# Kernel tuning notes

Hardware: AMD Instinct MI355X
Metric: run time of the kernel (lower is better)

Reference implementation:

```python
import jax, jax.numpy as jnp
import numpy as np

B, M, RPI = 16, 80, 256            # images, objects/image, relations/image
N, R = B * M, B * RPI
DF, REP, EMB, HID, NH, L = 12544, 1024, 256, 512, 8, 4
OBJC, RELC = 151, 51
IMW, IMH = 800.0, 600.0


def _ln(x, g, b):
    m = x.mean(-1, keepdims=True)
    v = ((x - m) ** 2).mean(-1, keepdims=True)
    return (x - m) * jax.lax.rsqrt(v + 1e-5) * g + b


def _encoder(x, qkv_w, qkv_b, out_w, out_b, f1_w, f1_b, f2_w, f2_b, ln1_s, ln1_b, ln2_s, ln2_b):
    # post-LN transformer encoder, L layers, x: [B, M, HID]
    Bb, Mm, D = x.shape
    dk = D // NH
    scale = 1.0 / jnp.sqrt(jnp.float32(dk))
    for l in range(L):
        qkv = x @ qkv_w[l].T + qkv_b[l]
        q, k, v = jnp.split(qkv, 3, axis=-1)
        hs = lambda t: t.reshape(Bb, Mm, NH, dk).transpose(0, 2, 1, 3)
        q, k, v = hs(q), hs(k), hs(v)
        att = jax.nn.softmax(jnp.einsum('bhqd,bhkd->bhqk', q, k) * scale, axis=-1)
        o = jnp.einsum('bhqk,bhkd->bhqd', att, v).transpose(0, 2, 1, 3).reshape(Bb, Mm, D)
        x = _ln(x + o @ out_w[l].T + out_b[l], ln1_s[l], ln1_b[l])
        f = jax.nn.relu(x @ f1_w[l].T + f1_b[l]) @ f2_w[l].T + f2_b[l]
        x = _ln(x + f, ln2_s[l], ln2_b[l])
    return x


def _box_info(boxes):
    wh = boxes[:, 2:] - boxes[:, :2] + 1.0
    xy = boxes[:, :2] + 0.5 * wh
    w, h = wh[:, :1], wh[:, 1:]
    x, y = xy[:, :1], xy[:, 1:]
    x1, y1, x2, y2 = boxes[:, 0:1], boxes[:, 1:2], boxes[:, 2:3], boxes[:, 3:4]
    return jnp.concatenate([w / IMW, h / IMH, x / IMW, y / IMH, x1 / IMW, y1 / IMH,
                            x2 / IMW, y2 / IMH, w * h / (IMW * IMH)], axis=-1)  # [N, 9]


def setup_inputs() -> dict:
    key = jax.random.key(0)
    ks = iter(jax.random.split(key, 80))
    nrm = lambda shape, s=0.02: jax.random.normal(next(ks), shape, jnp.float32) * s
    d = {}
    d['features'] = jax.random.normal(next(ks), (N, DF), jnp.float32)
    d['union_features'] = jax.random.normal(next(ks), (R, REP), jnp.float32)
    x1 = jax.random.uniform(next(ks), (N, 1)) * (IMW - 120.0)
    y1 = jax.random.uniform(next(ks), (N, 1)) * (IMH - 120.0)
    w = jax.random.uniform(next(ks), (N, 1)) * 100.0 + 5.0
    h = jax.random.uniform(next(ks), (N, 1)) * 100.0 + 5.0
    d['boxes'] = jnp.concatenate([x1, y1, x1 + w, y1 + h], axis=-1)
    d['logits'] = jax.random.normal(next(ks), (N, OBJC), jnp.float32)
    d['labels'] = jax.random.randint(next(ks), (N,), 0, OBJC)
    d['rel_pair_idxs'] = jax.random.randint(next(ks), (B, RPI, 2), 0, M)
    # feature extractor
    d['fe1_w'] = nrm((REP, DF)); d['fe1_b'] = jnp.zeros((REP,))
    d['fe2_w'] = nrm((REP, REP)); d['fe2_b'] = jnp.zeros((REP,))
    # embeddings
    d['emb1'] = nrm((OBJC, EMB), 1.0)
    d['emb2'] = nrm((OBJC, EMB), 1.0)
    # bbox embed 9->32->128
    d['bb1_w'] = nrm((32, 9)); d['bb1_b'] = jnp.zeros((32,))
    d['bb2_w'] = nrm((128, 32)); d['bb2_b'] = jnp.zeros((128,))
    d['lobj_w'] = nrm((HID, REP + EMB + 128)); d['lobj_b'] = jnp.zeros((HID,))
    d['ledge_w'] = nrm((HID, EMB + HID)); d['ledge_b'] = jnp.zeros((HID,))
    for p in ('o', 'e'):
        d[p + 'qkv_w'] = nrm((L, 3 * HID, HID)); d[p + 'qkv_b'] = jnp.zeros((L, 3 * HID))
        d[p + 'out_w'] = nrm((L, HID, HID)); d[p + 'out_b'] = jnp.zeros((L, HID))
        d[p + 'f1_w'] = nrm((L, HID, HID)); d[p + 'f1_b'] = jnp.zeros((L, HID))
        d[p + 'f2_w'] = nrm((L, HID, HID)); d[p + 'f2_b'] = jnp.zeros((L, HID))
        d[p + 'ln1_s'] = jnp.ones((L, HID)); d[p + 'ln1_b'] = jnp.zeros((L, HID))
        d[p + 'ln2_s'] = jnp.ones((L, HID)); d[p + 'ln2_b'] = jnp.zeros((L, HID))
    d['pcat_w'] = nrm((REP, 2 * HID)); d['pcat_b'] = jnp.zeros((REP,))
    d['fuse_w'] = nrm((REP, REP + HID)); d['fuse_b'] = jnp.zeros((REP,))
    d['cpx_w'] = nrm((RELC, 2 * REP)); d['cpx_b'] = jnp.zeros((RELC,))
    d['dpath_w'] = nrm((RELC, REP)); d['dpath_b'] = jnp.zeros((RELC,))
    return d


def reference(features, union_features, boxes, logits,
              fe1_w, fe1_b, fe2_w, fe2_b, emb1, emb2,
              bb1_w, bb1_b, bb2_w, bb2_b, lobj_w, lobj_b, ledge_w, ledge_b,
              oqkv_w, oqkv_b, oout_w, oout_b, of1_w, of1_b, of2_w, of2_b,
              oln1_s, oln1_b, oln2_s, oln2_b,
              eqkv_w, eqkv_b, eout_w, eout_b, ef1_w, ef1_b, ef2_w, ef2_b,
              eln1_s, eln1_b, eln2_s, eln2_b,
              pcat_w, pcat_b, fuse_w, fuse_b, cpx_w, cpx_b, dpath_w, dpath_b,
              labels, rel_pair_idxs):
    # FeatureExtractor
    bf = jax.nn.relu(features @ fe1_w.T + fe1_b)
    bf = jax.nn.relu(bf @ fe2_w.T + fe2_b)                        # [N, REP]
    # bbox embedding (dropout = identity in eval)
    pos = jax.nn.relu(_box_info(boxes) @ bb1_w.T + bb1_b)
    pos = jax.nn.relu(pos @ bb2_w.T + bb2_b)                      # [N, 128]
    obj_rep = jnp.concatenate([bf, emb1[labels], pos], -1) @ lobj_w.T + lobj_b  # [N, HID]
    obj_emb = _encoder(obj_rep.reshape(B, M, HID), oqkv_w, oqkv_b, oout_w, oout_b,
                       of1_w, of1_b, of2_w, of2_b, oln1_s, oln1_b, oln2_s, oln2_b)  # [B, M, HID]
    edge_in = jnp.concatenate([obj_emb.reshape(N, HID), emb2[labels]], -1) @ ledge_w.T + ledge_b
    gctx = _encoder(edge_in.reshape(B, M, HID), eqkv_w, eqkv_b, eout_w, eout_b,
                    ef1_w, ef1_b, ef2_w, ef2_b, eln1_s, eln1_b, eln2_s, eln2_b).mean(axis=1)  # [B, HID]
    # pair gather per image
    head = jax.vmap(lambda e, i: e[i])(obj_emb, rel_pair_idxs[:, :, 0])  # [B, RPI, HID]
    tail = jax.vmap(lambda e, i: e[i])(obj_emb, rel_pair_idxs[:, :, 1])
    pair = jnp.concatenate([head, tail], -1).reshape(R, 2 * HID)
    local = pair @ pcat_w.T + pcat_b                               # [R, REP]
    gexp = jnp.repeat(gctx, RPI, axis=0)                           # [R, HID]
    sem = jax.nn.relu(jnp.concatenate([local, gexp], -1) @ fuse_w.T + fuse_b)
    final = jnp.concatenate([sem, union_features], -1)             # [R, 2*REP]
    rel_logits = final @ cpx_w.T + cpx_b + local @ dpath_w.T + dpath_b  # [R, RELC]
    return rel_logits
```

## Files before the change

kernel.cpp:

```cpp
#include <hip/hip_runtime.h>
#include <hip/hip_bf16.h>
#include <cstdint>

#define DEV_INLINE __device__ __forceinline__

using u16 = unsigned short;
typedef __attribute__((ext_vector_type(8))) short bf8_t;
typedef __attribute__((ext_vector_type(4))) float f32x4;

constexpr int cB = 16, cM = 80, cRPI = 256;
constexpr int cN = cB * cM;
constexpr int cR = cB * cRPI;
constexpr int cDF = 12544, cREP = 1024, cEMB = 256, cHID = 512, cNH = 8, cL = 4;
constexpr int cRELC = 51;

DEV_INLINE u16 f2bf(float x) { return __builtin_bit_cast(u16, __float2bfloat16(x)); }
DEV_INLINE float bf2f(u16 u) { return __bfloat162float(__builtin_bit_cast(__hip_bfloat16, u)); }

DEV_INLINE float wave_max(float v) {
#pragma unroll
  for (int o = 32; o; o >>= 1) v = fmaxf(v, __shfl_xor(v, o));
  return v;
}
DEV_INLINE float wave_sum(float v) {
#pragma unroll
  for (int o = 32; o; o >>= 1) v += __shfl_xor(v, o);
  return v;
}

DEV_INLINE void xcd_remap(int& bx, int& by) {
  const int gx = gridDim.x;
  const int nwg = gx * gridDim.y;
  const int id = blockIdx.x + gx * blockIdx.y;
  const int q = nwg >> 3, r = nwg & 7;
  const int x = id & 7, k = id >> 3;
  const int idp = (x < r) ? x * (q + 1) + k : r * (q + 1) + (x - r) * q + k;
  bx = idp % gx;
  by = idp / gx;
}

template <int KK>
__global__ __launch_bounds__(256) void gemm_k1(
    const u16* __restrict__ A, int lda,
    const u16* __restrict__ Bw, int ldb,
    float* __restrict__ outF, int ldc,
    u16* __restrict__ outH, int ldh,
    const float* __restrict__ bias,
    const float* __restrict__ res, int resld, int resmode,
    int relu)
{
  constexpr int GR = KK / 8;
  constexpr int CH = 32 * GR;
  __shared__ u16 As[32 * KK];
  __shared__ u16 Bs[32 * KK];
  const int tid = threadIdx.x;
  const int wid = tid >> 6, lane = tid & 63;
  const int l15 = lane & 15, l4 = lane >> 4;
  int bx, by;
  xcd_remap(bx, by);
  const int bm = by * 32, bn = bx * 32;
  const int wr = wid >> 1, wc = wid & 1;

#pragma unroll
  for (int i = 0; i < CH / 256; ++i) {
    const int c = i * 256 + tid;
    const int row = c / GR, gran = c % GR;
    const int sg = gran ^ (row & 7);
    const u16* gp = A + (size_t)(bm + row) * lda + sg * 8;
    __builtin_amdgcn_global_load_lds(
        (const __attribute__((address_space(1))) void*)gp,
        (__attribute__((address_space(3))) void*)((char*)As + (size_t)(i * 256 + wid * 64) * 16),
        16, 0, 0);
  }
#pragma unroll
  for (int i = 0; i < CH / 256; ++i) {
    const int c = i * 256 + tid;
    const int row = c / GR, gran = c % GR;
    const int sg = gran ^ (row & 7);
    const u16* gp = Bw + (size_t)(bn + row) * ldb + sg * 8;
    __builtin_amdgcn_global_load_lds(
        (const __attribute__((address_space(1))) void*)gp,
        (__attribute__((address_space(3))) void*)((char*)Bs + (size_t)(i * 256 + wid * 64) * 16),
        16, 0, 0);
  }
  __syncthreads();

  const int ra = wr * 16 + l15;
  const int rb = wc * 16 + l15;
  f32x4 acc = {};
#pragma unroll
  for (int ks = 0; ks < KK / 32; ++ks) {
    const int ga = ((ks << 2) | l4) ^ (ra & 7);
    const int gb = ((ks << 2) | l4) ^ (rb & 7);
    const bf8_t af = *(const bf8_t*)&As[ra * KK + ga * 8];
    const bf8_t bv = *(const bf8_t*)&Bs[rb * KK + gb * 8];
    acc = __builtin_amdgcn_mfma_f32_16x16x32_bf16(af, bv, acc, 0, 0, 0);
  }

  const int ccol = bn + wc * 16 + l15;
  const float bv = bias ? bias[ccol] : 0.f;
#pragma unroll
  for (int g = 0; g < 4; ++g) {
    const int r = bm + wr * 16 + l4 * 4 + g;
    float v = acc[g] + bv;
    if (resmode == 1) v += res[(size_t)r * resld + ccol];
    else if (resmode == 2) v += res[(size_t)(r >> 8) * resld + ccol];
    if (relu) v = fmaxf(v, 0.f);
    if (outF) outF[(size_t)r * ldc + ccol] = v;
    if (outH) outH[(size_t)r * ldh + ccol] = f2bf(v);
  }
}

static void g512(hipStream_t s, const u16* A, int lda, const u16* W, int ldb,
                 int M, int N, float* outF, int ldc, u16* outH, int ldh,
                 const float* bias, const float* res, int resld, int resmode, int relu) {
  dim3 g(N / 32, M / 32);
  gemm_k1<512><<<g, 256, 0, s>>>(A, lda, W, ldb, outF, ldc, outH, ldh,
                                 bias, res, resld, resmode, relu);
}

template <int BM, int BN, bool SPLIT>
__global__ __launch_bounds__(256) void gemm_h(
    const u16* __restrict__ A, int lda,
    const u16* __restrict__ Bw, int ldb,
    int Mr, int Nr, int Klen,
    float* __restrict__ outF, int ldc,
    u16* __restrict__ outH, int ldh,
    const float* __restrict__ bias,
    const float* __restrict__ res, int resld, int resmode,
    int relu)
{
  constexpr int MF = BM > 32 ? BM / 32 : 1, NF = BN > 32 ? BN / 32 : 1;
  constexpr int ACH = BM * 4, BCH = BN * 4;
  __shared__ u16 As[2][BM * 32];
  __shared__ u16 Bs[2][BN * 32];
  const int tid = threadIdx.x;
  const int wid = tid >> 6, lane = tid & 63;
  const int l15 = lane & 15, l4 = lane >> 4;
  int bx, by;
  xcd_remap(bx, by);
  const int bm = by * BM, bn = bx * BN;
  const int wr = wid >> 1, wc = wid & 1;
  const int kbase = SPLIT ? blockIdx.z * Klen : 0;

  f32x4 acc[MF][NF] = {};

  auto stage = [&](int buf, int ks) {
    const int k0 = kbase + (ks << 5);
#pragma unroll
    for (int i = 0; i < (ACH + 255) / 256; ++i) {
      const int cA = i * 256 + tid;
      if (ACH % 256 == 0 || cA < ACH) {
        const int row = cA >> 2, seg = cA & 3;
        const int sseg = seg ^ (row & 3);
        const u16* gp = A + (size_t)(bm + row) * lda + k0 + sseg * 8;
        __builtin_amdgcn_global_load_lds(
            (const __attribute__((address_space(1))) void*)gp,
            (__attribute__((address_space(3))) void*)((char*)As[buf] + (size_t)(cA - lane) * 16),
            16, 0, 0);
      }
    }
#pragma unroll
    for (int i = 0; i < (BCH + 255) / 256; ++i) {
      const int cBp = i * 256 + ((tid + 128) & 255);
      if (BCH % 256 == 0 || cBp < BCH) {
        const int row = cBp >> 2, seg = cBp & 3;
        const int sseg = seg ^ (row & 3);
        int brow = bn + row; if (brow > Nr - 1) brow = Nr - 1;
        const u16* gp = Bw + (size_t)brow * ldb + k0 + sseg * 8;
        __builtin_amdgcn_global_load_lds(
            (const __attribute__((address_space(1))) void*)gp,
            (__attribute__((address_space(3))) void*)((char*)Bs[buf] + (size_t)(cBp - lane) * 16),
            16, 0, 0);
      }
    }
  };

  const int nk = Klen >> 5;
  stage(0, 0);
  __syncthreads();

  for (int ks = 0; ks < nk; ++ks) {
    const int cur = ks & 1;
    if (ks + 1 < nk) stage(cur ^ 1, ks + 1);

    bf8_t af[MF], bfr[NF];
#pragma unroll
    for (int m = 0; m < MF; ++m) {
      const int r = wr * (BM / 2) + m * 16 + l15;
      const int g = l4 ^ (r & 3);
      af[m] = *(const bf8_t*)&As[cur][r * 32 + g * 8];
    }
#pragma unroll
    for (int n = 0; n < NF; ++n) {
      const int r = wc * (BN / 2) + n * 16 + l15;
      const int g = l4 ^ (r & 3);
      bfr[n] = *(const bf8_t*)&Bs[cur][r * 32 + g * 8];
    }
#pragma unroll
    for (int m = 0; m < MF; ++m)
#pragma unroll
      for (int n = 0; n < NF; ++n)
        acc[m][n] = __builtin_amdgcn_mfma_f32_16x16x32_bf16(af[m], bfr[n], acc[m][n], 0, 0, 0);
    __syncthreads();
  }

  if (SPLIT) {
    float* po = outF + (size_t)blockIdx.z * Mr * ldc;
#pragma unroll
    for (int m = 0; m < MF; ++m)
#pragma unroll
      for (int n = 0; n < NF; ++n) {
        const int ccol = bn + wc * (BN / 2) + n * 16 + l15;
        if (ccol >= Nr) continue;
#pragma unroll
        for (int g = 0; g < 4; ++g) {
          const int r = bm + wr * (BM / 2) + m * 16 + l4 * 4 + g;
          po[(size_t)r * ldc + ccol] = acc[m][n][g];
        }
      }
  } else {
#pragma unroll
    for (int m = 0; m < MF; ++m)
#pragma unroll
      for (int n = 0; n < NF; ++n) {
        const int ccol = bn + wc * (BN / 2) + n * 16 + l15;
        if (ccol >= Nr) continue;
        const float bv = bias ? bias[ccol] : 0.f;
#pragma unroll
        for (int g = 0; g < 4; ++g) {
          const int r = bm + wr * (BM / 2) + m * 16 + l4 * 4 + g;
          float v = acc[m][n][g] + bv;
          if (resmode == 1) v += res[(size_t)r * resld + ccol];
          else if (resmode == 2) v += res[(size_t)(r >> 8) * resld + ccol];
          if (relu) v = fmaxf(v, 0.f);
          if (outF) outF[(size_t)r * ldc + ccol] = v;
          if (outH) outH[(size_t)r * ldh + ccol] = f2bf(v);
        }
      }
  }
}

template <int BM, int BN>
static void g16(hipStream_t s, const u16* A, int lda, const u16* W, int ldb,
                int M, int N, int K, float* outF, int ldc, u16* outH, int ldh,
                const float* bias, const float* res, int resld, int resmode, int relu) {
  dim3 g((N + BN - 1) / BN, M / BM);
  gemm_h<BM, BN, false><<<g, 256, 0, s>>>(A, lda, W, ldb, M, N, K, outF, ldc, outH, ldh,
                                          bias, res, resld, resmode, relu);
}

__global__ void conv_big2(const float* __restrict__ f, const float* __restrict__ w,
                          u16* __restrict__ fh, u16* __restrict__ wh) {
  constexpr int N1 = cN * cDF / 4;
  constexpr int N2 = cREP * cDF / 4;
  for (int i = blockIdx.x * 256 + threadIdx.x; i < N1 + N2; i += gridDim.x * 256) {
    const float4 v = (i < N1) ? ((const float4*)f)[i] : ((const float4*)w)[i - N1];
    ushort4 o = {f2bf(v.x), f2bf(v.y), f2bf(v.z), f2bf(v.w)};
    if (i < N1) ((ushort4*)fh)[i] = o; else ((ushort4*)wh)[i - N1] = o;
  }
}

constexpr size_t W_FE2 = 0, W_LOBJ = W_FE2 + 1048576, W_LEDGE = W_LOBJ + 720896,
  W_OQKV = W_LEDGE + 393216, W_OOUT = W_OQKV + 3145728, W_OF1 = W_OOUT + 1048576,
  W_OF2 = W_OF1 + 1048576, W_EQKV = W_OF2 + 1048576, W_EOUT = W_EQKV + 3145728,
  W_EF1 = W_EOUT + 1048576, W_EF2 = W_EF1 + 1048576, W_PCAT = W_EF2 + 1048576,
  W_FUSE = W_PCAT + 1048576, W_WEND = W_FUSE + 1572864;

struct EncSrcs {
  const float *fe2, *lobj, *ledge, *oqkv, *oout, *of1, *of2,
              *eqkv, *eout, *ef1, *ef2, *pcat, *fuse;
};

__global__ void conv_enc(EncSrcs S, u16* __restrict__ wb) {
#define SEG(nm, OFF, PRE, LEN) \
  if (i < (PRE) + (LEN)) { \
    const float4 v = ((const float4*)S.nm)[i - (PRE)]; \
    ushort4 o = {f2bf(v.x), f2bf(v.y), f2bf(v.z), f2bf(v.w)}; \
    ((ushort4*)(wb + (OFF)))[i - (PRE)] = o; \
  } else
  for (int i = blockIdx.x * 256 + threadIdx.x; i < (int)(W_WEND / 4); i += gridDim.x * 256) {
    SEG(fe2,  W_FE2,   0,       262144)
    SEG(lobj, W_LOBJ,  262144,  180224)
    SEG(ledge,W_LEDGE, 442368,  98304)
    SEG(oqkv, W_OQKV,  540672,  786432)
    SEG(oout, W_OOUT,  1327104, 262144)
    SEG(of1,  W_OF1,   1589248, 262144)
    SEG(of2,  W_OF2,   1851392, 262144)
    SEG(eqkv, W_EQKV,  2113536, 786432)
    SEG(eout, W_EOUT,  2899968, 262144)
    SEG(ef1,  W_EF1,   3162112, 262144)
    SEG(ef2,  W_EF2,   3424256, 262144)
    SEG(pcat, W_PCAT,  3686400, 262144)
    SEG(fuse, W_FUSE,  3948544, 393216)
    { }
  }
#undef SEG
}

__global__ void conv_cat(const float* __restrict__ cpx, const float* __restrict__ dpath,
                         const float* __restrict__ cb, const float* __restrict__ db,
                         u16* __restrict__ catw, float* __restrict__ biasc) {
  constexpr int N1 = cRELC * 512;
  constexpr int N2 = cRELC * 256;
  const int i0 = blockIdx.x * 256 + threadIdx.x;
  if (blockIdx.x == 0 && threadIdx.x < cRELC) biasc[threadIdx.x] = cb[threadIdx.x] + db[threadIdx.x];
  for (int i = i0; i < N1 + N2; i += gridDim.x * 256) {
    if (i < N1) {
      const int r = i >> 9, c = i & 511;
      const float4 v = ((const float4*)cpx)[i];
      ushort4 o = {f2bf(v.x), f2bf(v.y), f2bf(v.z), f2bf(v.w)};
      ((ushort4*)catw)[r * 768 + c] = o;
    } else {
      const int j = i - N1, r = j >> 8, c = j & 255;
      const float4 v = ((const float4*)dpath)[j];
      ushort4 o = {f2bf(v.x), f2bf(v.y), f2bf(v.z), f2bf(v.w)};
      ((ushort4*)catw)[r * 768 + 512 + c] = o;
    }
  }
}

__global__ void conv2d_kernel(const float* __restrict__ src, int slda,
                              u16* __restrict__ dst, int dld, int cols) {
  const int r = blockIdx.x;
  for (int c = threadIdx.x; c < cols; c += blockDim.x)
    dst[(size_t)r * dld + c] = f2bf(src[(size_t)r * slda + c]);
}

__global__ __launch_bounds__(256) void prep_obj(
    const float* __restrict__ boxes,
    const float* __restrict__ bb1w, const float* __restrict__ bb1b,
    const float* __restrict__ bb2w, const float* __restrict__ bb2b,
    const float* __restrict__ emb1, const int* __restrict__ labels,
    u16* __restrict__ obj_in) {
  __shared__ float W1[288];
  __shared__ float W2[4096];
  __shared__ float P1[8][33];
  const int tid = threadIdx.x;
  for (int i = tid; i < 288; i += 256) W1[i] = bb1w[i];
  for (int i = tid; i < 4096; i += 256) W2[i] = bb2w[i];
  __syncthreads();
  const int r8 = tid >> 5, sub = tid & 31;
  const int row = blockIdx.x * 8 + r8;
  const float x1 = boxes[row * 4], y1 = boxes[row * 4 + 1];
  const float x2 = boxes[row * 4 + 2], y2 = boxes[row * 4 + 3];
  const float w = x2 - x1 + 1.f, h = y2 - y1 + 1.f;
  const float bi[9] = {w / 800.f, h / 600.f, (x1 + 0.5f * w) / 800.f, (y1 + 0.5f * h) / 600.f,
                       x1 / 800.f, y1 / 600.f, x2 / 800.f, y2 / 600.f, w * h / 480000.f};
  float p = bb1b[sub];
#pragma unroll
  for (int j = 0; j < 9; ++j) p += bi[j] * W1[sub * 9 + j];
  P1[r8][sub] = fmaxf(p, 0.f);
  __syncthreads();
#pragma unroll
  for (int jo = 0; jo < 4; ++jo) {
    const int o = sub + jo * 32;
    float a = bb2b[o];
#pragma unroll
    for (int j2 = 0; j2 < 32; ++j2) a += P1[r8][j2] * W2[o * 32 + j2];
    obj_in[(size_t)row * 1408 + 1280 + o] = f2bf(fmaxf(a, 0.f));
  }
  const int l = labels[row];
#pragma unroll
  for (int k = 0; k < 8; ++k)
    obj_in[(size_t)row * 1408 + 1024 + sub + k * 32] = f2bf(emb1[(size_t)l * 256 + sub + k * 32]);
}

__global__ void gather_emb_h(const float* __restrict__ emb, const int* __restrict__ labels,
                             u16* __restrict__ dst, int dld) {
  const int i = blockIdx.x;
  const int l = labels[i];
  const float* s = emb + (size_t)l * cEMB;
  for (int c = threadIdx.x; c < cEMB; c += blockDim.x)
    dst[(size_t)i * dld + c] = f2bf(s[c]);
}

__global__ __launch_bounds__(256) void attn_kernel(const u16* __restrict__ qkv,
                                                   u16* __restrict__ o) {
  __shared__ float Ks[80][65];
  __shared__ float Vs[80][65];
  const int bh = blockIdx.x;
  const int b = bh >> 3, h = bh & 7;
  const int tid = threadIdx.x;
  const u16* base = qkv + (size_t)(b * cM) * 1536 + h * 64;

  for (int e = tid; e < 640; e += 256) {
    const int r = e >> 3, d0 = (e & 7) * 8;
    const bf8_t kv = *(const bf8_t*)&base[(size_t)r * 1536 + 512 + d0];
    const bf8_t vv = *(const bf8_t*)&base[(size_t)r * 1536 + 1024 + d0];
#pragma unroll
    for (int j = 0; j < 8; ++j) {
      Ks[r][d0 + j] = bf2f((u16)kv[j]);
      Vs[r][d0 + j] = bf2f((u16)vv[j]);
    }
  }
  __syncthreads();

  const int wave = tid >> 6, lane = tid & 63;
  const int r0 = blockIdx.y * 16;
  for (int r = r0 + wave; r < r0 + 16; r += 4) {
    const float qd = bf2f(base[(size_t)r * 1536 + lane]);
    const int c2 = 64 + lane;
    const int c2c = (c2 < 80) ? c2 : 0;
    float s0 = 0.f, s1 = 0.f;
#pragma unroll 8
    for (int d = 0; d < 64; ++d) {
      const float qv = __shfl(qd, d);
      s0 += qv * Ks[lane][d];
      s1 += qv * Ks[c2c][d];
    }
    s0 *= 0.125f;
    s1 = (c2 < 80) ? s1 * 0.125f : -1e30f;
    const float mx = wave_max(fmaxf(s0, s1));
    const float p0 = __expf(s0 - mx);
    const float p1 = (c2 < 80) ? __expf(s1 - mx) : 0.f;
    const float ssum = wave_sum(p0 + p1);

    float od = 0.f;
#pragma unroll 8
    for (int c = 0; c < 64; ++c) od += __shfl(p0, c) * Vs[c][lane];
#pragma unroll
    for (int c = 0; c < 16; ++c) od += __shfl(p1, c) * Vs[64 + c][lane];
    od /= ssum;
    o[(size_t)(b * cM + r) * cHID + h * 64 + lane] = f2bf(od);
  }
}

__global__ __launch_bounds__(256) void ln_kernel(
    const float* __restrict__ in, float* __restrict__ outF,
    u16* __restrict__ outH, int ldh,
    const float* __restrict__ g, const float* __restrict__ bta) {
  const int row = blockIdx.x * 4 + (threadIdx.x >> 6);
  const int lane = threadIdx.x & 63;
  const float* x = in + (size_t)row * cHID;
  float v[8];
  float s = 0.f;
#pragma unroll
  for (int i = 0; i < 8; ++i) { v[i] = x[lane + i * 64]; s += v[i]; }
  s = wave_sum(s);
  const float mean = s * (1.f / 512.f);
  float vs = 0.f;
#pragma unroll
  for (int i = 0; i < 8; ++i) { const float d = v[i] - mean; vs += d * d; }
  vs = wave_sum(vs);
  const float inv = rsqrtf(vs * (1.f / 512.f) + 1e-5f);
#pragma unroll
  for (int i = 0; i < 8; ++i) {
    const int c = lane + i * 64;
    const float y = (v[i] - mean) * inv * g[c] + bta[c];
    outF[(size_t)row * cHID + c] = y;
    outH[(size_t)row * ldh + c] = f2bf(y);
  }
}

__global__ void mean_kernel(const float* __restrict__ x, u16* __restrict__ gctx_h) {
  const int b = blockIdx.x;
  const int c = threadIdx.x;
  float s = 0.f;
  for (int m = 0; m < cM; ++m) s += x[(size_t)(b * cM + m) * cHID + c];
  gctx_h[(size_t)b * cHID + c] = f2bf(s * (1.f / 80.f));
}

__global__ void pair_gather_h(const u16* __restrict__ obj, int old, const int* __restrict__ idx,
                              u16* __restrict__ pair) {
  const int r = blockIdx.x;
  const int b = r >> 8, rr = r & 255;
  const int i0 = idx[(size_t)(b * cRPI + rr) * 2 + 0];
  const int i1 = idx[(size_t)(b * cRPI + rr) * 2 + 1];
  const u16* hsrc = obj + (size_t)(b * cM + i0) * old;
  const u16* tsrc = obj + (size_t)(b * cM + i1) * old;
  u16* p = pair + (size_t)r * 1024;
  for (int c = threadIdx.x; c < cHID; c += blockDim.x) {
    p[c] = hsrc[c];
    p[cHID + c] = tsrc[c];
  }
}

__global__ void reduce8_kernel(const float* __restrict__ p, const float* __restrict__ bias,
                               u16* __restrict__ outH) {
  const int idx = blockIdx.x * 256 + threadIdx.x;
  constexpr int total = cN * cREP;
  if (idx >= total) return;
  float v = bias[idx & 1023];
#pragma unroll
  for (int z = 0; z < 8; ++z) v += p[(size_t)z * total + idx];
  outH[idx] = f2bf(fmaxf(v, 0.f));
}

__global__ void freduce_kernel(const float* __restrict__ p, const float* __restrict__ biasc,
                               float* __restrict__ out) {
  const int idx = blockIdx.x * 256 + threadIdx.x;
  if (idx >= cR * cRELC) return;
  const int r = idx / cRELC, c = idx - r * cRELC;
  float v = biasc[c];
#pragma unroll
  for (int z = 0; z < 4; ++z) v += p[(size_t)z * cR * 64 + (size_t)r * 64 + c];
  out[idx] = v;
}

static void run_encoder(hipStream_t s, float* x, u16* xh, u16* qkvh, u16* attn_h,
                        float* res1, u16* f_h,
                        const u16* qkvw, const float* qkvb,
                        const u16* outw, const float* outb,
                        const u16* f1w, const float* f1b,
                        const u16* f2w, const float* f2b,
                        const float* ln1s, const float* ln1b,
                        const float* ln2s, const float* ln2b,
                        u16* last_bf, int last_ld) {
  for (int l = 0; l < cL; ++l) {
    g512(s, xh, 512, qkvw + (size_t)l * 1536 * 512, 512, cN, 1536,
         nullptr, 0, qkvh, 1536, qkvb + l * 1536, nullptr, 0, 0, 0);
    attn_kernel<<<dim3(cB * cNH, 5), 256, 0, s>>>(qkvh, attn_h);
    g512(s, attn_h, 512, outw + (size_t)l * 512 * 512, 512, cN, 512,
         res1, 512, nullptr, 0, outb + l * 512, x, 512, 1, 0);
    ln_kernel<<<cN / 4, 256, 0, s>>>(res1, x, xh, 512, ln1s + l * 512, ln1b + l * 512);
    g512(s, xh, 512, f1w + (size_t)l * 512 * 512, 512, cN, 512,
         nullptr, 0, f_h, 512, f1b + l * 512, nullptr, 0, 0, 1);
    g512(s, f_h, 512, f2w + (size_t)l * 512 * 512, 512, cN, 512,
         res1, 512, nullptr, 0, f2b + l * 512, x, 512, 1, 0);
    const bool last = (l == cL - 1);
    ln_kernel<<<cN / 4, 256, 0, s>>>(res1, x, last ? last_bf : xh, last ? last_ld : 512,
                                     ln2s + l * 512, ln2b + l * 512);
  }
}

constexpr size_t OFF_FEAT  = 0;
constexpr size_t OFF_FE1W  = 32112640;
constexpr size_t OFF_PART  = 57802752;
constexpr size_t P_END     = 99745792;
constexpr size_t OFF_PAIR  = 0;
constexpr size_t OFF_FINAL = 8388608;
constexpr size_t OFF_OBJIN = 33554432;
constexpr size_t OFF_QKVH  = 37158912;
constexpr size_t OFF_X     = 41091072;
constexpr size_t OFF_XH    = 43712512;
constexpr size_t OFF_ATTN  = 45023232;
constexpr size_t OFF_RES   = 46333952;
constexpr size_t OFF_FH    = 48955392;
constexpr size_t OFF_EDGE  = 50266112;

extern "C" void kernel_launch(void* const* d_in, const int* in_sizes, int n_in,
                              void* d_out, int out_size, void* d_ws, size_t ws_size,
                              hipStream_t stream) {
  (void)in_sizes; (void)n_in; (void)out_size; (void)ws_size;

  const float* features = (const float*)d_in[0];
  const float* unionf   = (const float*)d_in[1];
  const float* boxes    = (const float*)d_in[2];
  const int*   labels   = (const int*)d_in[4];
  const int*   relidx   = (const int*)d_in[5];
  const float* fe1_w = (const float*)d_in[6];
  const float* fe1_b = (const float*)d_in[7];
  const float* fe2_w = (const float*)d_in[8];
  const float* fe2_b = (const float*)d_in[9];
  const float* emb1  = (const float*)d_in[10];
  const float* emb2  = (const float*)d_in[11];
  const float* bb1_w = (const float*)d_in[12];
  const float* bb1_b = (const float*)d_in[13];
  const float* bb2_w = (const float*)d_in[14];
  const float* bb2_b = (const float*)d_in[15];
  const float* lobj_w = (const float*)d_in[16];
  const float* lobj_b = (const float*)d_in[17];
  const float* ledge_w = (const float*)d_in[18];
  const float* ledge_b = (const float*)d_in[19];
  const float* oqkv_w = (const float*)d_in[20];
  const float* oqkv_b = (const float*)d_in[21];
  const float* oout_w = (const float*)d_in[22];
  const float* oout_b = (const float*)d_in[23];
  const float* of1_w = (const float*)d_in[24];
  const float* of1_b = (const float*)d_in[25];
  const float* of2_w = (const float*)d_in[26];
  const float* of2_b = (const float*)d_in[27];
  const float* oln1_s = (const float*)d_in[28];
  const float* oln1_b = (const float*)d_in[29];
  const float* oln2_s = (const float*)d_in[30];
  const float* oln2_b = (const float*)d_in[31];
  const float* eqkv_w = (const float*)d_in[32];
  const float* eqkv_b = (const float*)d_in[33];
  const float* eout_w = (const float*)d_in[34];
  const float* eout_b = (const float*)d_in[35];
  const float* ef1_w = (const float*)d_in[36];
  const float* ef1_b = (const float*)d_in[37];
  const float* ef2_w = (const float*)d_in[38];
  const float* ef2_b = (const float*)d_in[39];
  const float* eln1_s = (const float*)d_in[40];
  const float* eln1_b = (const float*)d_in[41];
  const float* eln2_s = (const float*)d_in[42];
  const float* eln2_b = (const float*)d_in[43];
  const float* pcat_w = (const float*)d_in[44];
  const float* pcat_b = (const float*)d_in[45];
  const float* fuse_w = (const float*)d_in[46];
  const float* fuse_b = (const float*)d_in[47];
  const float* cpx_w  = (const float*)d_in[48];
  const float* cpx_b  = (const float*)d_in[49];
  const float* dpath_w = (const float*)d_in[50];
  const float* dpath_b = (const float*)d_in[51];

  char* wsb = (char*)d_ws;
  u16* feat_h  = (u16*)(wsb + OFF_FEAT);
  u16* fe1w_h  = (u16*)(wsb + OFF_FE1W);
  float* part  = (float*)(wsb + OFF_PART);
  u16* pair    = (u16*)(wsb + OFF_PAIR);
  u16* finalb  = (u16*)(wsb + OFF_FINAL);
  u16* obj_in  = (u16*)(wsb + OFF_OBJIN);
  u16* qkvh    = (u16*)(wsb + OFF_QKVH);
  float* x     = (float*)(wsb + OFF_X);
  u16* xh      = (u16*)(wsb + OFF_XH);
  u16* attn_h  = (u16*)(wsb + OFF_ATTN);
  float* res1  = (float*)(wsb + OFF_RES);
  u16* f_h     = (u16*)(wsb + OFF_FH);
  u16* edge_in = (u16*)(wsb + OFF_EDGE);

  size_t off = P_END;
  auto alloc = [&](size_t bytes) { char* p = wsb + off; off = (off + bytes + 255) & ~(size_t)255; return p; };
  u16* wblock   = (u16*)alloc(W_WEND * 2);
  u16* catw     = (u16*)alloc(313344);
  float* biasc  = (float*)alloc(256);
  u16* bf0h     = (u16*)alloc(2621440);
  u16* gctx_h   = (u16*)alloc(65536);
  float* gcproj = (float*)alloc(262144);
  float* fpart  = (float*)alloc(4194304);

  const u16* fe2w_h   = wblock + W_FE2;
  const u16* lobjw_h  = wblock + W_LOBJ;
  const u16* ledgew_h = wblock + W_LEDGE;
  const u16* oqkvw_h  = wblock + W_OQKV;
  const u16* ooutw_h  = wblock + W_OOUT;
  const u16* of1w_h   = wblock + W_OF1;
  const u16* of2w_h   = wblock + W_OF2;
  const u16* eqkvw_h  = wblock + W_EQKV;
  const u16* eoutw_h  = wblock + W_EOUT;
  const u16* ef1w_h   = wblock + W_EF1;
  const u16* ef2w_h   = wblock + W_EF2;
  const u16* pcatw_h  = wblock + W_PCAT;
  const u16* fusew_h  = wblock + W_FUSE;

  conv_big2<<<2048, 256, 0, stream>>>(features, fe1_w, feat_h, fe1w_h);
  EncSrcs es = {fe2_w, lobj_w, ledge_w, oqkv_w, oout_w, of1_w, of2_w,
                eqkv_w, eout_w, ef1_w, ef2_w, pcat_w, fuse_w};
  conv_enc<<<2048, 256, 0, stream>>>(es, wblock);
  conv_cat<<<160, 256, 0, stream>>>(cpx_w, dpath_w, cpx_b, dpath_b, catw, biasc);

  gemm_h<128, 128, true><<<dim3(8, 10, 8), 256, 0, stream>>>(
      feat_h, cDF, fe1w_h, cDF, cN, cREP, cDF / 8, part, cREP,
      nullptr, 0, nullptr, nullptr, 0, 0, 0);
  reduce8_kernel<<<(cN * cREP + 255) / 256, 256, 0, stream>>>(part, fe1_b, bf0h);

  prep_obj<<<cN / 8, 256, 0, stream>>>(boxes, bb1_w, bb1_b, bb2_w, bb2_b, emb1, labels, obj_in);

  g16<32, 32>(stream, bf0h, 1024, fe2w_h, 1024, cN, cREP, cREP,
              nullptr, 0, obj_in, 1408, fe2_b, nullptr, 0, 0, 1);

  g16<32, 32>(stream, obj_in, 1408, lobjw_h, 1408, cN, cHID, 1408,
              x, 512, xh, 512, lobj_b, nullptr, 0, 0, 0);

  run_encoder(stream, x, xh, qkvh, attn_h, res1, f_h,
              oqkvw_h, oqkv_b, ooutw_h, oout_b, of1w_h, of1_b, of2w_h, of2_b,
              oln1_s, oln1_b, oln2_s, oln2_b, edge_in, 768);

  gather_emb_h<<<cN, 256, 0, stream>>>(emb2, labels, edge_in + 512, 768);
  pair_gather_h<<<cR, 256, 0, stream>>>(edge_in, 768, relidx, pair);

  g16<32, 32>(stream, edge_in, 768, ledgew_h, 768, cN, cHID, 768,
              x, 512, xh, 512, ledge_b, nullptr, 0, 0, 0);
  run_encoder(stream, x, xh, qkvh, attn_h, res1, f_h,
              eqkvw_h, eqkv_b, eoutw_h, eout_b, ef1w_h, ef1_b, ef2w_h, ef2_b,
              eln1_s, eln1_b, eln2_s, eln2_b, xh, 512);
  mean_kernel<<<cB, cHID, 0, stream>>>(x, gctx_h);

  g512(stream, gctx_h, 512, fusew_h + 1024, 1536, 64, cREP,
       gcproj, 1024, nullptr, 0, fuse_b, nullptr, 0, 0, 0);

  conv2d_kernel<<<cR, 256, 0, stream>>>(unionf, 1024, finalb + 1024, 3072, 1024);
  g16<128, 64>(stream, pair, 1024, pcatw_h, 1024, cR, cREP, 1024,
               nullptr, 0, finalb + 2048, 3072, pcat_b, nullptr, 0, 0, 0);
  g16<128, 64>(stream, finalb + 2048, 3072, fusew_h, 1536, cR, cREP, 1024,
               nullptr, 0, finalb, 3072, nullptr, gcproj, 1024, 2, 1);

  gemm_h<64, 64, true><<<dim3(1, 64, 4), 256, 0, stream>>>(
      finalb, 3072, catw, 3072, cR, cRELC, 3072 / 4, fpart, 64,
      nullptr, 0, nullptr, nullptr, 0, 0, 0);
  freduce_kernel<<<(cR * cRELC + 255) / 256, 256, 0, stream>>>(fpart, biasc, (float*)d_out);
}
```

Baseline: 879.7 us.

## Fuse encoder out-proj, LN1, FFN, LN2 and next-layer QKV into one kernel

Replaces the per-layer sequence of out-projection GEMM, two LayerNorm kernels, two FFN GEMMs and the next layer's QKV GEMM with a single enc_tail kernel. Each block owns 32 full rows and keeps activations in LDS across the chained GEMMs, computing LayerNorm stats in-register. This removes several launches and round trips of intermediates through global memory. In exchange only 40 blocks run, each streaming all weights, so it has far less parallelism than the separate tiled GEMMs.

```diff
diff --git a/kernel.cpp b/kernel.cpp
--- a/kernel.cpp
+++ b/kernel.cpp
@@ -26,6 +26,12 @@
 #pragma unroll
   for (int o = 32; o; o >>= 1) v += __shfl_xor(v, o);
   return v;
+}
+
+DEV_INLINE void gl_lds16(const u16* gp, char* lp) {
+  __builtin_amdgcn_global_load_lds(
+      (const __attribute__((address_space(1))) void*)gp,
+      (__attribute__((address_space(3))) void*)lp, 16, 0, 0);
 }
 
 DEV_INLINE void xcd_remap(int& bx, int& by) {
@@ -37,6 +43,211 @@
   const int idp = (x < r) ? x * (q + 1) + k : r * (q + 1) + (x - r) * q + k;
   bx = idp % gx;
   by = idp / gx;
+}
+
+struct TailArgs {
+  const u16* attn;
+  float* x;
+  const u16* outw; const float* outb;
+  const u16* f1w;  const float* f1b;
+  const u16* f2w;  const float* f2b;
+  const float *ln1s, *ln1b, *ln2s, *ln2b;
+  const u16* qkvw; const float* qkvb;
+  u16* qkvh;
+  u16* last_bf; int last_ld;
+  int is_last;
+};
+
+__global__ __launch_bounds__(256, 1) void enc_tail(TailArgs A) {
+  __shared__ u16 SA[32 * 512];
+  __shared__ u16 SW[2][512 * 32];
+  __shared__ float redS[32][4], redQ[32][4], stat[32][2];
+
+  const int tid = threadIdx.x;
+  const int wid = tid >> 6, lane = tid & 63;
+  const int l15 = lane & 15, l4 = lane >> 4;
+  const int bm = blockIdx.x * 32;
+
+#pragma unroll
+  for (int i = 0; i < 8; ++i) {
+    const int slot = i * 256 + tid;
+    const int row = slot >> 6, g = slot & 63;
+    const int sg = (g & ~7) | ((g ^ row) & 7);
+    gl_lds16(A.attn + (size_t)(bm + row) * 512 + sg * 8,
+             (char*)SA + (size_t)(i * 256 + wid * 64) * 16);
+  }
+
+  f32x4 acc[2][8];
+  float z[2][8][4];
+
+  auto runGemm = [&](const u16* W, int nbase) {
+#pragma unroll
+    for (int m = 0; m < 2; ++m)
+#pragma unroll
+      for (int f = 0; f < 8; ++f) acc[m][f] = f32x4{0.f, 0.f, 0.f, 0.f};
+
+    auto stageW = [&](int buf, int chunk) {
+#pragma unroll
+      for (int i = 0; i < 8; ++i) {
+        const int slot = i * 256 + tid;
+        const int row = slot >> 2, g = slot & 3;
+        const int sg = g ^ (row & 3);
+        gl_lds16(W + (size_t)(nbase + row) * 512 + chunk * 32 + sg * 8,
+                 (char*)SW[buf] + (size_t)(i * 256 + wid * 64) * 16);
+      }
+    };
+    stageW(0, 0);
+    __syncthreads();
+    for (int chunk = 0; chunk < 16; ++chunk) {
+      const int cur = chunk & 1;
+      if (chunk + 1 < 16) stageW(cur ^ 1, chunk + 1);
+      bf8_t af[2];
+#pragma unroll
+      for (int m = 0; m < 2; ++m) {
+        const int ra = m * 16 + l15;
+        const int gg = chunk * 4 + l4;
+        const int sg = (gg & ~7) | ((gg ^ ra) & 7);
+        af[m] = *(const bf8_t*)&SA[ra * 512 + sg * 8];
+      }
+#pragma unroll
+      for (int f = 0; f < 8; ++f) {
+        const int rb = wid * 128 + f * 16 + l15;
+        const int gb = l4 ^ (rb & 3);
+        const bf8_t bv = *(const bf8_t*)&SW[cur][rb * 32 + gb * 8];
+#pragma unroll
+        for (int m = 0; m < 2; ++m)
+          acc[m][f] = __builtin_amdgcn_mfma_f32_16x16x32_bf16(af[m], bv, acc[m][f], 0, 0, 0);
+      }
+      __syncthreads();
+    }
+  };
+
+  auto lnStats = [&]() {
+#pragma unroll
+    for (int m = 0; m < 2; ++m)
+#pragma unroll
+      for (int g = 0; g < 4; ++g) {
+        float sm = 0.f, q = 0.f;
+#pragma unroll
+        for (int f = 0; f < 8; ++f) { const float t = acc[m][f][g]; sm += t; q += t * t; }
+#pragma unroll
+        for (int o = 1; o < 16; o <<= 1) { sm += __shfl_xor(sm, o); q += __shfl_xor(q, o); }
+        if (l15 == 0) {
+          const int rl = m * 16 + l4 * 4 + g;
+          redS[rl][wid] = sm; redQ[rl][wid] = q;
+        }
+      }
+    __syncthreads();
+    if (tid < 32) {
+      const float sm = redS[tid][0] + redS[tid][1] + redS[tid][2] + redS[tid][3];
+      const float q  = redQ[tid][0] + redQ[tid][1] + redQ[tid][2] + redQ[tid][3];
+      const float mean = sm * (1.f / 512.f);
+      stat[tid][0] = mean;
+      stat[tid][1] = rsqrtf(q * (1.f / 512.f) - mean * mean + 1e-5f);
+    }
+    __syncthreads();
+  };
+
+  runGemm(A.outw, 0);
+#pragma unroll
+  for (int m = 0; m < 2; ++m)
+#pragma unroll
+    for (int f = 0; f < 8; ++f) {
+      const int col = wid * 128 + f * 16 + l15;
+      const float bv = A.outb[col];
+#pragma unroll
+      for (int g = 0; g < 4; ++g) {
+        const int R = bm + m * 16 + l4 * 4 + g;
+        acc[m][f][g] += bv + A.x[(size_t)R * 512 + col];
+      }
+    }
+
+  lnStats();
+#pragma unroll
+  for (int m = 0; m < 2; ++m)
+#pragma unroll
+    for (int f = 0; f < 8; ++f) {
+      const int col = wid * 128 + f * 16 + l15;
+      const float s1 = A.ln1s[col], b1 = A.ln1b[col];
+#pragma unroll
+      for (int g = 0; g < 4; ++g) {
+        const int rl = m * 16 + l4 * 4 + g;
+        const float y = (acc[m][f][g] - stat[rl][0]) * stat[rl][1] * s1 + b1;
+        z[m][f][g] = y;
+        const int g0 = col >> 3;
+        const int sg = (g0 & ~7) | ((g0 ^ rl) & 7);
+        SA[rl * 512 + sg * 8 + (col & 7)] = f2bf(y);
+      }
+    }
+
+  runGemm(A.f1w, 0);
+#pragma unroll
+  for (int m = 0; m < 2; ++m)
+#pragma unroll
+    for (int f = 0; f < 8; ++f) {
+      const int col = wid * 128 + f * 16 + l15;
+      const float bv = A.f1b[col];
+#pragma unroll
+      for (int g = 0; g < 4; ++g) {
+        const int rl = m * 16 + l4 * 4 + g;
+        const float y = fmaxf(acc[m][f][g] + bv, 0.f);
+        const int g0 = col >> 3;
+        const int sg = (g0 & ~7) | ((g0 ^ rl) & 7);
+        SA[rl * 512 + sg * 8 + (col & 7)] = f2bf(y);
+      }
+    }
+
+  runGemm(A.f2w, 0);
+#pragma unroll
+  for (int m = 0; m < 2; ++m)
+#pragma unroll
+    for (int f = 0; f < 8; ++f) {
+      const int col = wid * 128 + f * 16 + l15;
+      const float bv = A.f2b[col];
+#pragma unroll
+      for (int g = 0; g < 4; ++g)
+        acc[m][f][g] += bv + z[m][f][g];
+    }
+  lnStats();
+#pragma unroll
+  for (int m = 0; m < 2; ++m)
+#pragma unroll
+    for (int f = 0; f < 8; ++f) {
+      const int col = wid * 128 + f * 16 + l15;
+      const float s2 = A.ln2s[col], b2 = A.ln2b[col];
+#pragma unroll
+      for (int g = 0; g < 4; ++g) {
+        const int rl = m * 16 + l4 * 4 + g;
+        const int R = bm + rl;
+        const float y = (acc[m][f][g] - stat[rl][0]) * stat[rl][1] * s2 + b2;
+        A.x[(size_t)R * 512 + col] = y;
+        if (A.is_last) {
+          A.last_bf[(size_t)R * A.last_ld + col] = f2bf(y);
+        } else {
+          const int g0 = col >> 3;
+          const int sg = (g0 & ~7) | ((g0 ^ rl) & 7);
+          SA[rl * 512 + sg * 8 + (col & 7)] = f2bf(y);
+        }
+      }
+    }
+
+  if (!A.is_last) {
+    for (int p = 0; p < 3; ++p) {
+      runGemm(A.qkvw, p * 512);
+#pragma unroll
+      for (int m = 0; m < 2; ++m)
+#pragma unroll
+        for (int f = 0; f < 8; ++f) {
+          const int col = p * 512 + wid * 128 + f * 16 + l15;
+          const float bv = A.qkvb[col];
+#pragma unroll
+          for (int g = 0; g < 4; ++g) {
+            const int R = bm + m * 16 + l4 * 4 + g;
+            A.qkvh[(size_t)R * 1536 + col] = f2bf(acc[m][f][g] + bv);
+          }
+        }
+    }
+  }
 }
 
 template <int KK>
@@ -66,22 +277,16 @@
     const int c = i * 256 + tid;
     const int row = c / GR, gran = c % GR;
     const int sg = gran ^ (row & 7);
-    const u16* gp = A + (size_t)(bm + row) * lda + sg * 8;
-    __builtin_amdgcn_global_load_lds(
-        (const __attribute__((address_space(1))) void*)gp,
-        (__attribute__((address_space(3))) void*)((char*)As + (size_t)(i * 256 + wid * 64) * 16),
-        16, 0, 0);
+    gl_lds16(A + (size_t)(bm + row) * lda + sg * 8,
+             (char*)As + (size_t)(i * 256 + wid * 64) * 16);
   }
 #pragma unroll
   for (int i = 0; i < CH / 256; ++i) {
     const int c = i * 256 + tid;
     const int row = c / GR, gran = c % GR;
     const int sg = gran ^ (row & 7);
-    const u16* gp = Bw + (size_t)(bn + row) * ldb + sg * 8;
-    __builtin_amdgcn_global_load_lds(
-        (const __attribute__((address_space(1))) void*)gp,
-        (__attribute__((address_space(3))) void*)((char*)Bs + (size_t)(i * 256 + wid * 64) * 16),
-        16, 0, 0);
+    gl_lds16(Bw + (size_t)(bn + row) * ldb + sg * 8,
+             (char*)Bs + (size_t)(i * 256 + wid * 64) * 16);
   }
   __syncthreads();
 
@@ -153,11 +358,8 @@
       if (ACH % 256 == 0 || cA < ACH) {
         const int row = cA >> 2, seg = cA & 3;
         const int sseg = seg ^ (row & 3);
-        const u16* gp = A + (size_t)(bm + row) * lda + k0 + sseg * 8;
-        __builtin_amdgcn_global_load_lds(
-            (const __attribute__((address_space(1))) void*)gp,
-            (__attribute__((address_space(3))) void*)((char*)As[buf] + (size_t)(cA - lane) * 16),
-            16, 0, 0);
+        gl_lds16(A + (size_t)(bm + row) * lda + k0 + sseg * 8,
+                 (char*)As[buf] + (size_t)(cA - lane) * 16);
       }
     }
 #pragma unroll
@@ -167,11 +369,8 @@
         const int row = cBp >> 2, seg = cBp & 3;
         const int sseg = seg ^ (row & 3);
         int brow = bn + row; if (brow > Nr - 1) brow = Nr - 1;
-        const u16* gp = Bw + (size_t)brow * ldb + k0 + sseg * 8;
-        __builtin_amdgcn_global_load_lds(
-            (const __attribute__((address_space(1))) void*)gp,
-            (__attribute__((address_space(3))) void*)((char*)Bs[buf] + (size_t)(cBp - lane) * 16),
-            16, 0, 0);
+        gl_lds16(Bw + (size_t)brow * ldb + k0 + sseg * 8,
+                 (char*)Bs[buf] + (size_t)(cBp - lane) * 16);
       }
     }
   };
@@ -426,33 +625,6 @@
   }
 }
 
-__global__ __launch_bounds__(256) void ln_kernel(
-    const float* __restrict__ in, float* __restrict__ outF,
-    u16* __restrict__ outH, int ldh,
-    const float* __restrict__ g, const float* __restrict__ bta) {
-  const int row = blockIdx.x * 4 + (threadIdx.x >> 6);
-  const int lane = threadIdx.x & 63;
-  const float* x = in + (size_t)row * cHID;
-  float v[8];
-  float s = 0.f;
-#pragma unroll
-  for (int i = 0; i < 8; ++i) { v[i] = x[lane + i * 64]; s += v[i]; }
-  s = wave_sum(s);
-  const float mean = s * (1.f / 512.f);
-  float vs = 0.f;
-#pragma unroll
-  for (int i = 0; i < 8; ++i) { const float d = v[i] - mean; vs += d * d; }
-  vs = wave_sum(vs);
-  const float inv = rsqrtf(vs * (1.f / 512.f) + 1e-5f);
-#pragma unroll
-  for (int i = 0; i < 8; ++i) {
-    const int c = lane + i * 64;
-    const float y = (v[i] - mean) * inv * g[c] + bta[c];
-    outF[(size_t)row * cHID + c] = y;
-    outH[(size_t)row * ldh + c] = f2bf(y);
-  }
-}
-
 __global__ void mean_kernel(const float* __restrict__ x, u16* __restrict__ gctx_h) {
   const int b = blockIdx.x;
   const int c = threadIdx.x;
@@ -499,7 +671,6 @@
 }
 
 static void run_encoder(hipStream_t s, float* x, u16* xh, u16* qkvh, u16* attn_h,
-                        float* res1, u16* f_h,
                         const u16* qkvw, const float* qkvb,
                         const u16* outw, const float* outb,
                         const u16* f1w, const float* f1b,
@@ -507,20 +678,24 @@
                         const float* ln1s, const float* ln1b,
                         const float* ln2s, const float* ln2b,
                         u16* last_bf, int last_ld) {
+  g512(s, xh, 512, qkvw, 512, cN, 1536, nullptr, 0, qkvh, 1536, qkvb,
+       nullptr, 0, 0, 0);
   for (int l = 0; l < cL; ++l) {
-    g512(s, xh, 512, qkvw + (size_t)l * 1536 * 512, 512, cN, 1536,
-         nullptr, 0, qkvh, 1536, qkvb + l * 1536, nullptr, 0, 0, 0);
     attn_kernel<<<dim3(cB * cNH, 5), 256, 0, s>>>(qkvh, attn_h);
-    g512(s, attn_h, 512, outw + (size_t)l * 512 * 512, 512, cN, 512,
-         res1, 512, nullptr, 0, outb + l * 512, x, 512, 1, 0);
-    ln_kernel<<<cN / 4, 256, 0, s>>>(res1, x, xh, 512, ln1s + l * 512, ln1b + l * 512);
-    g512(s, xh, 512, f1w + (size_t)l * 512 * 512, 512, cN, 512,
-         nullptr, 0, f_h, 512, f1b + l * 512, nullptr, 0, 0, 1);
-    g512(s, f_h, 512, f2w + (size_t)l * 512 * 512, 512, cN, 512,
-         res1, 512, nullptr, 0, f2b + l * 512, x, 512, 1, 0);
+    TailArgs a;
+    a.attn = attn_h; a.x = x;
+    a.outw = outw + (size_t)l * 512 * 512; a.outb = outb + l * 512;
+    a.f1w = f1w + (size_t)l * 512 * 512;   a.f1b = f1b + l * 512;
+    a.f2w = f2w + (size_t)l * 512 * 512;   a.f2b = f2b + l * 512;
+    a.ln1s = ln1s + l * 512; a.ln1b = ln1b + l * 512;
+    a.ln2s = ln2s + l * 512; a.ln2b = ln2b + l * 512;
     const bool last = (l == cL - 1);
-    ln_kernel<<<cN / 4, 256, 0, s>>>(res1, x, last ? last_bf : xh, last ? last_ld : 512,
-                                     ln2s + l * 512, ln2b + l * 512);
+    a.qkvw = last ? nullptr : qkvw + (size_t)(l + 1) * 1536 * 512;
+    a.qkvb = last ? nullptr : qkvb + (l + 1) * 1536;
+    a.qkvh = qkvh;
+    a.last_bf = last_bf; a.last_ld = last_ld;
+    a.is_last = last ? 1 : 0;
+    enc_tail<<<cN / 32, 256, 0, s>>>(a);
   }
 }
 
@@ -535,8 +710,6 @@
 constexpr size_t OFF_X     = 41091072;
 constexpr size_t OFF_XH    = 43712512;
 constexpr size_t OFF_ATTN  = 45023232;
-constexpr size_t OFF_RES   = 46333952;
-constexpr size_t OFF_FH    = 48955392;
 constexpr size_t OFF_EDGE  = 50266112;
 
 extern "C" void kernel_launch(void* const* d_in, const int* in_sizes, int n_in,
@@ -607,8 +780,6 @@
   float* x     = (float*)(wsb + OFF_X);
   u16* xh      = (u16*)(wsb + OFF_XH);
   u16* attn_h  = (u16*)(wsb + OFF_ATTN);
-  float* res1  = (float*)(wsb + OFF_RES);
-  u16* f_h     = (u16*)(wsb + OFF_FH);
   u16* edge_in = (u16*)(wsb + OFF_EDGE);
 
   size_t off = P_END;
@@ -624,14 +795,6 @@
   const u16* fe2w_h   = wblock + W_FE2;
   const u16* lobjw_h  = wblock + W_LOBJ;
   const u16* ledgew_h = wblock + W_LEDGE;
-  const u16* oqkvw_h  = wblock + W_OQKV;
-  const u16* ooutw_h  = wblock + W_OOUT;
-  const u16* of1w_h   = wblock + W_OF1;
-  const u16* of2w_h   = wblock + W_OF2;
-  const u16* eqkvw_h  = wblock + W_EQKV;
-  const u16* eoutw_h  = wblock + W_EOUT;
-  const u16* ef1w_h   = wblock + W_EF1;
-  const u16* ef2w_h   = wblock + W_EF2;
   const u16* pcatw_h  = wblock + W_PCAT;
   const u16* fusew_h  = wblock + W_FUSE;
 
@@ -654,8 +817,9 @@
   g16<32, 32>(stream, obj_in, 1408, lobjw_h, 1408, cN, cHID, 1408,
               x, 512, xh, 512, lobj_b, nullptr, 0, 0, 0);
 
-  run_encoder(stream, x, xh, qkvh, attn_h, res1, f_h,
-              oqkvw_h, oqkv_b, ooutw_h, oout_b, of1w_h, of1_b, of2w_h, of2_b,
+  run_encoder(stream, x, xh, qkvh, attn_h,
+              wblock + W_OQKV, oqkv_b, wblock + W_OOUT, oout_b,
+              wblock + W_OF1, of1_b, wblock + W_OF2, of2_b,
               oln1_s, oln1_b, oln2_s, oln2_b, edge_in, 768);
 
   gather_emb_h<<<cN, 256, 0, stream>>>(emb2, labels, edge_in + 512, 768);
@@ -663,8 +827,9 @@
 
   g16<32, 32>(stream, edge_in, 768, ledgew_h, 768, cN, cHID, 768,
               x, 512, xh, 512, ledge_b, nullptr, 0, 0, 0);
-  run_encoder(stream, x, xh, qkvh, attn_h, res1, f_h,
-              eqkvw_h, eqkv_b, eoutw_h, eout_b, ef1w_h, ef1_b, ef2w_h, ef2_b,
+  run_encoder(stream, x, xh, qkvh, attn_h,
+              wblock + W_EQKV, eqkv_b, wblock + W_EOUT, eout_b,
+              wblock + W_EF1, ef1_b, wblock + W_EF2, ef2_b,
               eln1_s, eln1_b, eln2_s, eln2_b, xh, 512);
   mean_kernel<<<cB, cHID, 0, stream>>>(x, gctx_h);
 
```

Measured after the change: 1.138 ms. +29.4%, slower.
